# Kernel tuning notes

Hardware: AMD Instinct MI355X
Metric: run time of the kernel (lower is better)

The kernel has to match this reference:

```python
import jax, jax.numpy as jnp
import numpy as np

N = 100_000          # nodes
E = 1_600_000        # edges (avg degree 16)
F_RAW = 124          # float feature columns (after id column removed)
ID_DIM = 4
NF = F_RAW + ID_DIM  # encoder input features = 128
EMB = 64             # embedding_size, heads=1
L = 4                # num_layers
VOCAB = 2048         # id embedding table size
GAT_SLOPE = 0.2      # GATv2 attention leaky slope (PyG default)
ACT_SLOPE = 0.01     # nn.LeakyReLU default
EPS = 1e-5           # GraphNorm eps


def setup_inputs() -> dict:
    key = jax.random.key(0)
    ks = jax.random.split(key, 12)
    x_feat = jax.random.normal(ks[0], (N, F_RAW), jnp.float32)
    node_ids = jax.random.randint(ks[1], (N,), 0, VOCAB)
    edge_index = jax.random.randint(ks[2], (2, E), 0, N)
    emb_table = jax.random.normal(ks[3], (VOCAB, ID_DIM), jnp.float32) * 0.1
    w_in = jax.random.normal(ks[4], (NF, EMB), jnp.float32) / np.sqrt(NF)
    b_in = jnp.zeros((EMB,), jnp.float32)
    lin_w = jax.random.normal(ks[5], (L, EMB, EMB), jnp.float32) / np.sqrt(EMB)
    lin_b = jnp.zeros((L, EMB), jnp.float32)
    att = jax.random.normal(ks[6], (L, EMB), jnp.float32) / np.sqrt(EMB)
    conv_b = jnp.zeros((L, EMB), jnp.float32)
    gn_w = jnp.ones((L, EMB), jnp.float32)
    gn_b = jnp.zeros((L, EMB), jnp.float32)
    gn_ms = jnp.ones((L, EMB), jnp.float32)  # GraphNorm mean_scale
    return {"x_feat": x_feat, "node_ids": node_ids, "edge_index": edge_index,
            "emb_table": emb_table, "w_in": w_in, "b_in": b_in,
            "lin_w": lin_w, "lin_b": lin_b, "att": att, "conv_b": conv_b,
            "gn_w": gn_w, "gn_b": gn_b, "gn_ms": gn_ms}


def reference(x_feat, node_ids, edge_index, emb_table, w_in, b_in,
              lin_w, lin_b, att, conv_b, gn_w, gn_b, gn_ms):
    # id_encode: embedding lookup + concat with float features
    x = jnp.concatenate([x_feat, emb_table[node_ids]], axis=1)  # [N, 128]
    # encoder input projection (BatchNorm skipped: remove_random=True)
    x = jax.nn.leaky_relu(x @ w_in + b_in, ACT_SLOPE)           # [N, 64]
    n = x.shape[0]
    loops = jnp.arange(n)
    src = jnp.concatenate([edge_index[0], loops])               # add self loops
    dst = jnp.concatenate([edge_index[1], loops])
    h = None
    xs = []
    for l in range(L):
        # GATv2Conv, heads=1, share_weights=True (one shared linear)
        g = x @ lin_w[l] + lin_b[l]                             # [N, 64]
        e = jax.nn.leaky_relu(g[src] + g[dst], GAT_SLOPE) @ att[l]  # [E+N]
        # segment softmax over incoming edges per target node
        m = jax.ops.segment_max(e, dst, num_segments=n)
        ee = jnp.exp(e - m[dst])
        s = jax.ops.segment_sum(ee, dst, num_segments=n)
        alpha = ee / s[dst]                                     # [E+N]
        xs.append(alpha)
        x = jax.ops.segment_sum(alpha[:, None] * g[src], dst, num_segments=n) + conv_b[l]
        # GraphNorm (single graph: batch=None)
        mean = jnp.mean(x, axis=0)
        out = x - mean * gn_ms[l]
        var = jnp.mean(out * out, axis=0)
        x = out / jnp.sqrt(var + EPS) * gn_w[l] + gn_b[l]
        x = jax.nn.leaky_relu(x, ACT_SLOPE)
        # dropout p=0.3 is identity at inference
        h = x * 0.5 if h is None else h + x * 0.5
    return x, h, jnp.stack(xs, axis=0)  # ([N,64], [N,64], [L, E+N])
```

## Files before the change

### kernel.cpp

```cpp
#include <hip/hip_runtime.h>
#include <hip/hip_bf16.h>
#include <cstdint>

typedef __hip_bfloat16 bf16;
#define DEVI __device__ __forceinline__

DEVI float b2f(bf16 v){ return __bfloat162float(v); }
DEVI bf16 f2b(float v){ return __float2bfloat16(v); }
DEVI float lrelu(float x, float s){ return x > 0.f ? x : x * s; }

DEVI float ldf(const void* p, size_t i, int f){
  return f ? b2f(((const bf16*)p)[i]) : ((const float*)p)[i];
}
DEVI void stf(void* p, size_t i, int f, float v){
  if(f) ((bf16*)p)[i] = f2b(v); else ((float*)p)[i] = v;
}

DEVI float wave_sum(float v){
#pragma unroll
  for(int o = 32; o > 0; o >>= 1) v += __shfl_xor(v, o, 64);
  return v;
}
DEVI float qsum(float v){
  v += __shfl_xor(v, 1, 64);
  v += __shfl_xor(v, 2, 64);
  v += __shfl_xor(v, 4, 64);
  v += __shfl_xor(v, 8, 64);
  return v;
}

__global__ void k_detect(const uint32_t* __restrict__ xf, int* flag){
  const int lane = threadIdx.x & 63;
  float cnt = 0.f;
  for(int i = lane; i < 256; i += 64){
    uint32_t e = (xf[i] >> 7) & 0xFF;
    if(e >= 100 && e <= 140) cnt += 1.f;
  }
  cnt = wave_sum(cnt);
  if(lane == 0 && blockIdx.x == 0) *flag = (cnt > 180.f) ? 1 : 0;
}

__global__ __launch_bounds__(256) void k_encoder(
    const void* __restrict__ xf, const int* __restrict__ ids,
    const void* __restrict__ emb, const void* __restrict__ win,
    const void* __restrict__ bin, float* __restrict__ x,
    const int* __restrict__ flagp, int N)
{
  __shared__ float W[128*64];
  __shared__ float B[64];
  __shared__ float XR[4][128];
  const int t = threadIdx.x;
  const int f = *flagp;
  for(int i = t; i < 128*64; i += 256) W[i] = ldf(win, i, f);
  if(t < 64) B[t] = ldf(bin, t, f);
  __syncthreads();
  const int w = t >> 6, lane = t & 63;
  for(int base = blockIdx.x*4; base < N; base += gridDim.x*4){
    const int node = base + w;
    if(node < N){
      for(int k = lane; k < 128; k += 64){
        float v;
        if(k < 124) v = ldf(xf, (size_t)node*124 + k, f);
        else        v = ldf(emb, (size_t)ids[node]*4 + (k-124), f);
        XR[w][k] = v;
      }
      float acc = B[lane];
#pragma unroll 8
      for(int k = 0; k < 128; k++) acc = fmaf(XR[w][k], W[k*64+lane], acc);
      x[(size_t)node*64 + lane] = lrelu(acc, 0.01f);
    }
  }
}

__global__ __launch_bounds__(256) void k_linear(
    const float* __restrict__ x, const void* __restrict__ lw,
    const void* __restrict__ lb, float* __restrict__ g,
    const int* __restrict__ flagp, int layer, int N)
{
  __shared__ float W[64*64];
  __shared__ float B[64];
  __shared__ float XR[4][64];
  const int t = threadIdx.x;
  const int f = *flagp;
  const size_t wofs = (size_t)layer*64*64, bofs = (size_t)layer*64;
  for(int i = t; i < 64*64; i += 256) W[i] = ldf(lw, wofs + i, f);
  if(t < 64) B[t] = ldf(lb, bofs + t, f);
  __syncthreads();
  const int w = t >> 6, lane = t & 63;
  for(int base = blockIdx.x*4; base < N; base += gridDim.x*4){
    const int node = base + w;
    if(node < N){
      XR[w][lane] = x[(size_t)node*64 + lane];
      float acc = B[lane];
#pragma unroll 8
      for(int k = 0; k < 64; k++) acc = fmaf(XR[w][k], W[k*64+lane], acc);
      g[(size_t)node*64 + lane] = acc;
    }
  }
}

__global__ void k_deg_init(int* deg, float* stats, int N){
  int i = blockIdx.x*blockDim.x + threadIdx.x;
  if(i < N) deg[i] = 1;
  if(i < 4096) stats[i] = 0.f;
}
__global__ void k_deg_count(const int* __restrict__ dst, int* deg, int E){
  int j = blockIdx.x*blockDim.x + threadIdx.x;
  if(j < E) atomicAdd(&deg[dst[j]], 1);
}
__global__ __launch_bounds__(256) void k_scan_partial(const int* __restrict__ deg, int* partial, int N){
  __shared__ int red[256];
  const int c = blockIdx.x, base = c*1024, t = threadIdx.x;
  int s = 0;
  for(int i = t; i < 1024; i += 256){ int idx = base+i; s += (idx < N) ? deg[idx] : 0; }
  red[t] = s; __syncthreads();
  for(int o = 128; o > 0; o >>= 1){ if(t < o) red[t] += red[t+o]; __syncthreads(); }
  if(t == 0) partial[c] = red[0];
}
__global__ __launch_bounds__(256) void k_scan_final(
    const int* __restrict__ deg, const int* __restrict__ partial,
    int* __restrict__ off, int* __restrict__ cur, int N, int nchunks)
{
  __shared__ int vals[1024];
  __shared__ int tsum[256];
  __shared__ int red[256];
  const int c = blockIdx.x, base = c*1024, t = threadIdx.x;
  red[t] = (t < c && t < nchunks) ? partial[t] : 0;
  for(int i = t; i < 1024; i += 256){ int idx = base+i; vals[i] = (idx < N) ? deg[idx] : 0; }
  __syncthreads();
  for(int o = 128; o > 0; o >>= 1){ if(t < o) red[t] += red[t+o]; __syncthreads(); }
  const int cbase = red[0];
  int a0 = vals[t*4], a1 = vals[t*4+1], a2 = vals[t*4+2], a3 = vals[t*4+3];
  int s = a0+a1+a2+a3;
  tsum[t] = s; __syncthreads();
  for(int o = 1; o < 256; o <<= 1){
    int v = (t >= o) ? tsum[t-o] : 0;
    __syncthreads();
    tsum[t] += v;
    __syncthreads();
  }
  int excl = tsum[t] - s + cbase;
  int o0 = excl, o1 = o0+a0, o2 = o1+a1, o3 = o2+a2;
  int idx = base + t*4;
  if(idx   < N){ off[idx]   = o0; cur[idx]   = o0; }
  if(idx+1 < N){ off[idx+1] = o1; cur[idx+1] = o1; }
  if(idx+2 < N){ off[idx+2] = o2; cur[idx+2] = o2; }
  if(idx+3 < N){ off[idx+3] = o3; cur[idx+3] = o3; }
}
__global__ void k_scatter(const int* __restrict__ src, const int* __restrict__ dst,
                          int* cur, int* __restrict__ pos, int* __restrict__ csrc,
                          int E, int N){
  int j = blockIdx.x*blockDim.x + threadIdx.x;
  int T = E + N;
  if(j >= T) return;
  int s, d;
  if(j < E){ s = src[j]; d = dst[j]; } else { s = j - E; d = s; }
  int p = atomicAdd(&cur[d], 1);
  csrc[p] = s;
  pos[j]  = p;
}

__global__ __launch_bounds__(256) void k_gat(
    const float* __restrict__ g, const int* __restrict__ off,
    const int* __restrict__ deg, const int* __restrict__ csrc,
    const void* __restrict__ att, const void* __restrict__ convb,
    float* __restrict__ xout, float* __restrict__ acsr,
    float* __restrict__ stats, const int* __restrict__ flagp,
    int layer, int N)
{
  __shared__ float sv[4][64], sv2[4][64];
  const int t = threadIdx.x, w = t >> 6, lane = t & 63;
  const int q = lane >> 4, L = lane & 15;
  const int f = *flagp;
  const size_t pofs = (size_t)layer*64;
  float* __restrict__ st = stats + (size_t)layer*1024;
  const int node = blockIdx.x*4 + w;
  const bool act = node < N;
  const int nc = act ? node : (N-1);

  float4 attv, cbv;
  attv.x = ldf(att, pofs + 4*L+0, f); attv.y = ldf(att, pofs + 4*L+1, f);
  attv.z = ldf(att, pofs + 4*L+2, f); attv.w = ldf(att, pofs + 4*L+3, f);
  cbv.x = ldf(convb, pofs + 4*L+0, f); cbv.y = ldf(convb, pofs + 4*L+1, f);
  cbv.z = ldf(convb, pofs + 4*L+2, f); cbv.w = ldf(convb, pofs + 4*L+3, f);

  const float4 gd = *(const float4*)(g + (size_t)nc*64 + 4*L);
  const int o = off[nc];
  const int d = act ? deg[nc] : 0;
  const int sreg = csrc[o + (lane < d ? lane : 0)];

  float m = -1e30f, sp = 0.f, ereg = -1e30f;
  float4 acc = {0.f, 0.f, 0.f, 0.f};
  const int nit = (d + 3) >> 2;

  float4 gs;
  {
    const int s0 = __shfl(sreg, q, 64);
    gs = *(const float4*)(g + (size_t)s0*64 + 4*L);
  }
  for(int i = 0; i < nit; i++){
    float4 gnx = {0.f, 0.f, 0.f, 0.f};
    const int i1 = i + 1;
    const bool more = i1 < nit;
    if(more){
      int sn;
      if(i1 < 16) sn = __shfl(sreg, i1*4 + q, 64);
      else { const int j2 = i1*4 + q; sn = csrc[o + (j2 < d ? j2 : 0)]; }
      gnx = *(const float4*)(g + (size_t)sn*64 + 4*L);
    }
    const int j = i*4 + q;
    const bool have = j < d;
    float pe = lrelu(gs.x+gd.x, 0.2f)*attv.x + lrelu(gs.y+gd.y, 0.2f)*attv.y
             + lrelu(gs.z+gd.z, 0.2f)*attv.z + lrelu(gs.w+gd.w, 0.2f)*attv.w;
    float e = qsum(pe);
    if(!have) e = -1e30f;
    ereg = (L == i) ? e : ereg;
    const float mn = fmaxf(m, e);
    const float sc = __expf(m - mn);
    const float wt = __expf(e - mn);
    sp    = sp*sc    + wt;
    acc.x = acc.x*sc + wt*gs.x;
    acc.y = acc.y*sc + wt*gs.y;
    acc.z = acc.z*sc + wt*gs.z;
    acc.w = acc.w*sc + wt*gs.w;
    m = mn;
    if(more) gs = gnx;
  }
#pragma unroll
  for(int ofs = 16; ofs <= 32; ofs <<= 1){
    const float m2  = __shfl_xor(m,  ofs, 64);
    const float sp2 = __shfl_xor(sp, ofs, 64);
    float4 a2;
    a2.x = __shfl_xor(acc.x, ofs, 64); a2.y = __shfl_xor(acc.y, ofs, 64);
    a2.z = __shfl_xor(acc.z, ofs, 64); a2.w = __shfl_xor(acc.w, ofs, 64);
    const float mn = fmaxf(m, m2);
    const float sA = __expf(m - mn), sB = __expf(m2 - mn);
    sp    = sp*sA    + sp2*sB;
    acc.x = acc.x*sA + a2.x*sB;
    acc.y = acc.y*sA + a2.y*sB;
    acc.z = acc.z*sA + a2.z*sB;
    acc.w = acc.w*sA + a2.w*sB;
    m = mn;
  }
  const float inv = 1.f / sp;

  if(act){
    const int j = 4*L + q;
    if(j < d && j < 64)
      acsr[o + j] = __expf(ereg - m) * inv;
    for(int i = 16; i < nit; i++){
      const int j2 = i*4 + q;
      const bool have = j2 < d;
      const int s = csrc[o + (have ? j2 : 0)];
      const float4 gs2 = *(const float4*)(g + (size_t)s*64 + 4*L);
      float pe = lrelu(gs2.x+gd.x, 0.2f)*attv.x + lrelu(gs2.y+gd.y, 0.2f)*attv.y
               + lrelu(gs2.z+gd.z, 0.2f)*attv.z + lrelu(gs2.w+gd.w, 0.2f)*attv.w;
      float e = qsum(pe);
      if(have && L == 0)
        acsr[o + j2] = __expf(e - m) * inv;
    }
  }
  float4 v4 = {0.f, 0.f, 0.f, 0.f};
  if(act){
    v4.x = acc.x*inv + cbv.x; v4.y = acc.y*inv + cbv.y;
    v4.z = acc.z*inv + cbv.z; v4.w = acc.w*inv + cbv.w;
    if(q == 0) *(float4*)(xout + (size_t)node*64 + 4*L) = v4;
  }
  if(q == 0){
    sv [w][4*L+0] = v4.x;      sv [w][4*L+1] = v4.y;
    sv [w][4*L+2] = v4.z;      sv [w][4*L+3] = v4.w;
    sv2[w][4*L+0] = v4.x*v4.x; sv2[w][4*L+1] = v4.y*v4.y;
    sv2[w][4*L+2] = v4.z*v4.z; sv2[w][4*L+3] = v4.w*v4.w;
  }
  __syncthreads();
  if(w == 0){
    float a = sv[0][lane]+sv[1][lane]+sv[2][lane]+sv[3][lane];
    float b = sv2[0][lane]+sv2[1][lane]+sv2[2][lane]+sv2[3][lane];
    const int bank = (blockIdx.x & 7) * 128;
    atomicAdd(&st[bank + lane],      a);
    atomicAdd(&st[bank + 64 + lane], b);
  }
}

__global__ __launch_bounds__(256) void k_gn_apply(
    float* __restrict__ x, const float* __restrict__ stats,
    const void* __restrict__ gw, const void* __restrict__ gb,
    const void* __restrict__ gms, void* __restrict__ out,
    const float* __restrict__ acsr, const int* __restrict__ pos,
    size_t x_base, size_t h_base, size_t alpha_base,
    const int* __restrict__ flagp, int N, int T, int layer, float invN)
{
  const int f = *flagp;
  const int lane = threadIdx.x & 63;
  const float* __restrict__ st = stats + (size_t)layer*1024;
  const size_t pofs = (size_t)layer*64;
  float s1 = 0.f, s2 = 0.f;
#pragma unroll
  for(int c = 0; c < 8; c++){
    s1 += st[c*128 + lane];
    s2 += st[c*128 + 64 + lane];
  }
  const float mean = s1 * invN;
  const float ex2  = s2 * invN;
  const float c    = mean * ldf(gms, pofs + lane, f);
  const float var  = ex2 - 2.f*c*mean + c*c;
  const float a    = ldf(gw, pofs + lane, f) / sqrtf(var + 1e-5f);
  const float bb   = ldf(gb, pofs + lane, f);
  const size_t total = (size_t)N * 64;
  for(size_t idx = (size_t)blockIdx.x*256 + threadIdx.x; idx < total;
      idx += (size_t)gridDim.x*256){
    float v = (x[idx] - c) * a + bb;
    v = lrelu(v, 0.01f);
    x[idx] = v;
    float hv = 0.5f*v + (layer == 0 ? 0.f : ldf(out, h_base + idx, f));
    stf(out, h_base + idx, f, hv);
    if(layer == 3) stf(out, x_base + idx, f, v);
  }
  for(size_t j = (size_t)blockIdx.x*256 + threadIdx.x; j < (size_t)T;
      j += (size_t)gridDim.x*256){
    stf(out, alpha_base + j, f, acsr[pos[j]]);
  }
}

extern "C" void kernel_launch(void* const* d_in, const int* in_sizes, int n_in,
                              void* d_out, int out_size, void* d_ws, size_t ws_size,
                              hipStream_t stream) {
  const void* xf   = d_in[0];
  const int*  ids  = (const int*)d_in[1];
  const int*  eidx = (const int*)d_in[2];
  const void* emb  = d_in[3];
  const void* win  = d_in[4];
  const void* bin  = d_in[5];
  const void* lw   = d_in[6];
  const void* lb   = d_in[7];
  const void* att  = d_in[8];
  const void* cb   = d_in[9];
  const void* gw   = d_in[10];
  const void* gb   = d_in[11];
  const void* gms  = d_in[12];

  const int N = in_sizes[1];
  const int E = in_sizes[2] / 2;
  const int T = E + N;
  const int* srcp = eidx;
  const int* dstp = eidx + E;

  char* p = (char*)d_ws;
  float* x  = (float*)p; p += (size_t)N*64*4;
  float* g  = (float*)p; p += (size_t)N*64*4;
  int* deg  = (int*)p;   p += ((size_t)N*4 + 63) & ~63ull;
  int* off  = (int*)p;   p += ((size_t)N*4 + 63) & ~63ull;
  int* cur  = (int*)p;   p += ((size_t)N*4 + 63) & ~63ull;
  int* pos  = (int*)p;   p += ((size_t)T*4 + 63) & ~63ull;
  int* csrc = (int*)p;   p += ((size_t)T*4 + 63) & ~63ull;
  float* acsr = (float*)p; p += ((size_t)T*4 + 63) & ~63ull;
  int* partial = (int*)p; p += 4096;
  float* stats = (float*)p; p += 4*1024*4;
  int* flag = (int*)p;   p += 64;

  const size_t x_base = 0;
  const size_t h_base = (size_t)N*64;
  const size_t a_base = (size_t)2*N*64;

  k_detect<<<1, 64, 0, stream>>>((const uint32_t*)xf, flag);
  k_encoder<<<2048, 256, 0, stream>>>(xf, ids, emb, win, bin, x, flag, N);

  k_deg_init <<<(N+255)/256, 256, 0, stream>>>(deg, stats, N);
  k_deg_count<<<(E+255)/256, 256, 0, stream>>>(dstp, deg, E);
  const int nchunks = (N + 1023) / 1024;
  k_scan_partial<<<nchunks, 256, 0, stream>>>(deg, partial, N);
  k_scan_final  <<<nchunks, 256, 0, stream>>>(deg, partial, off, cur, N, nchunks);
  k_scatter     <<<(T+255)/256, 256, 0, stream>>>(srcp, dstp, cur, pos, csrc, E, N);

  for(int l = 0; l < 4; l++){
    k_linear<<<2048, 256, 0, stream>>>(x, lw, lb, g, flag, l, N);
    k_gat<<<(N+3)/4, 256, 0, stream>>>(g, off, deg, csrc, att, cb, x,
                                       acsr, stats, flag, l, N);
    k_gn_apply<<<1024, 256, 0, stream>>>(x, stats, gw, gb, gms, d_out,
                                         acsr, pos, x_base, h_base,
                                         a_base + (size_t)l*T, flag,
                                         N, T, l, 1.0f/(float)N);
  }
}
```

Baseline: 1.149 ms.

## Fuse GraphNorm apply into next layer's linear and deepen GAT gather prefetch

Moves the previous layer's GraphNorm normalization, activation, h accumulation and alpha scatter into the following layer's linear kernel. A separate final kernel handles the last layer. This removes a read-modify-write pass over x per layer and three kernel launches. The GAT kernel also prefetches source features two iterations ahead instead of one, to hide gather latency at the cost of extra registers.

New measurement: 1.073 ms. 1.07x faster.

```diff
diff --git a/kernel.cpp b/kernel.cpp
--- a/kernel.cpp
+++ b/kernel.cpp
@@ -75,7 +75,11 @@
 __global__ __launch_bounds__(256) void k_linear(
     const float* __restrict__ x, const void* __restrict__ lw,
     const void* __restrict__ lb, float* __restrict__ g,
-    const int* __restrict__ flagp, int layer, int N)
+    const float* __restrict__ stats, const void* __restrict__ gw,
+    const void* __restrict__ gb, const void* __restrict__ gms,
+    void* __restrict__ out, const float* __restrict__ acsr,
+    const int* __restrict__ pos, size_t h_base, size_t alpha_base,
+    const int* __restrict__ flagp, int layer, int N, int T, float invN)
 {
   __shared__ float W[64*64];
   __shared__ float B[64];
@@ -85,17 +89,43 @@
   const size_t wofs = (size_t)layer*64*64, bofs = (size_t)layer*64;
   for(int i = t; i < 64*64; i += 256) W[i] = ldf(lw, wofs + i, f);
   if(t < 64) B[t] = ldf(lb, bofs + t, f);
+  const int w = t >> 6, lane = t & 63;
+  float c = 0.f, a = 1.f, bb = 0.f;
+  if(layer > 0){
+    const int pl = layer - 1;
+    const float* __restrict__ st = stats + (size_t)pl*1024;
+    const size_t pofs = (size_t)pl*64;
+    float s1 = 0.f, s2 = 0.f;
+#pragma unroll
+    for(int k = 0; k < 8; k++){ s1 += st[k*128 + lane]; s2 += st[k*128 + 64 + lane]; }
+    const float mean = s1*invN, ex2 = s2*invN;
+    c = mean * ldf(gms, pofs + lane, f);
+    const float var = ex2 - 2.f*c*mean + c*c;
+    a = ldf(gw, pofs + lane, f) / sqrtf(var + 1e-5f);
+    bb = ldf(gb, pofs + lane, f);
+  }
   __syncthreads();
-  const int w = t >> 6, lane = t & 63;
   for(int base = blockIdx.x*4; base < N; base += gridDim.x*4){
     const int node = base + w;
     if(node < N){
-      XR[w][lane] = x[(size_t)node*64 + lane];
+      const size_t idx = (size_t)node*64 + lane;
+      float v = x[idx];
+      if(layer > 0){
+        v = lrelu((v - c)*a + bb, 0.01f);
+        float hv = 0.5f*v + (layer == 1 ? 0.f : ldf(out, h_base + idx, f));
+        stf(out, h_base + idx, f, hv);
+      }
+      XR[w][lane] = v;
       float acc = B[lane];
 #pragma unroll 8
       for(int k = 0; k < 64; k++) acc = fmaf(XR[w][k], W[k*64+lane], acc);
-      g[(size_t)node*64 + lane] = acc;
+      g[idx] = acc;
     }
+  }
+  if(layer > 0){
+    for(size_t j = (size_t)blockIdx.x*256 + threadIdx.x; j < (size_t)T;
+        j += (size_t)gridDim.x*256)
+      stf(out, alpha_base + j, f, acsr[pos[j]]);
   }
 }
 
@@ -193,21 +223,26 @@
   float4 acc = {0.f, 0.f, 0.f, 0.f};
   const int nit = (d + 3) >> 2;
 
-  float4 gs;
+  float4 gsA = {0.f,0.f,0.f,0.f}, gsB = {0.f,0.f,0.f,0.f};
   {
     const int s0 = __shfl(sreg, q, 64);
-    gs = *(const float4*)(g + (size_t)s0*64 + 4*L);
+    gsA = *(const float4*)(g + (size_t)s0*64 + 4*L);
+  }
+  if(nit > 1){
+    const int s1 = __shfl(sreg, 4 + q, 64);
+    gsB = *(const float4*)(g + (size_t)s1*64 + 4*L);
   }
   for(int i = 0; i < nit; i++){
     float4 gnx = {0.f, 0.f, 0.f, 0.f};
-    const int i1 = i + 1;
-    const bool more = i1 < nit;
-    if(more){
+    const int i2 = i + 2;
+    const bool more2 = i2 < nit;
+    if(more2){
       int sn;
-      if(i1 < 16) sn = __shfl(sreg, i1*4 + q, 64);
-      else { const int j2 = i1*4 + q; sn = csrc[o + (j2 < d ? j2 : 0)]; }
+      if(i2 < 16) sn = __shfl(sreg, i2*4 + q, 64);
+      else { const int j2 = i2*4 + q; sn = csrc[o + (j2 < d ? j2 : 0)]; }
       gnx = *(const float4*)(g + (size_t)sn*64 + 4*L);
     }
+    const float4 gs = gsA;
     const int j = i*4 + q;
     const bool have = j < d;
     float pe = lrelu(gs.x+gd.x, 0.2f)*attv.x + lrelu(gs.y+gd.y, 0.2f)*attv.y
@@ -224,7 +259,8 @@
     acc.z = acc.z*sc + wt*gs.z;
     acc.w = acc.w*sc + wt*gs.w;
     m = mn;
-    if(more) gs = gnx;
+    gsA = gsB;
+    if(more2) gsB = gnx;
   }
 #pragma unroll
   for(int ofs = 16; ofs <= 32; ofs <<= 1){
@@ -282,18 +318,18 @@
   }
 }
 
-__global__ __launch_bounds__(256) void k_gn_apply(
-    float* __restrict__ x, const float* __restrict__ stats,
+__global__ __launch_bounds__(256) void k_gn_final(
+    const float* __restrict__ x, const float* __restrict__ stats,
     const void* __restrict__ gw, const void* __restrict__ gb,
     const void* __restrict__ gms, void* __restrict__ out,
     const float* __restrict__ acsr, const int* __restrict__ pos,
     size_t x_base, size_t h_base, size_t alpha_base,
-    const int* __restrict__ flagp, int N, int T, int layer, float invN)
+    const int* __restrict__ flagp, int N, int T, float invN)
 {
   const int f = *flagp;
   const int lane = threadIdx.x & 63;
-  const float* __restrict__ st = stats + (size_t)layer*1024;
-  const size_t pofs = (size_t)layer*64;
+  const float* __restrict__ st = stats + (size_t)3*1024;
+  const size_t pofs = (size_t)3*64;
   float s1 = 0.f, s2 = 0.f;
 #pragma unroll
   for(int c = 0; c < 8; c++){
@@ -311,10 +347,9 @@
       idx += (size_t)gridDim.x*256){
     float v = (x[idx] - c) * a + bb;
     v = lrelu(v, 0.01f);
-    x[idx] = v;
-    float hv = 0.5f*v + (layer == 0 ? 0.f : ldf(out, h_base + idx, f));
+    float hv = 0.5f*v + ldf(out, h_base + idx, f);
     stf(out, h_base + idx, f, hv);
-    if(layer == 3) stf(out, x_base + idx, f, v);
+    stf(out, x_base + idx, f, v);
   }
   for(size_t j = (size_t)blockIdx.x*256 + threadIdx.x; j < (size_t)T;
       j += (size_t)gridDim.x*256){
@@ -361,6 +396,7 @@
   const size_t x_base = 0;
   const size_t h_base = (size_t)N*64;
   const size_t a_base = (size_t)2*N*64;
+  const float invN = 1.0f/(float)N;
 
   k_detect<<<1, 64, 0, stream>>>((const uint32_t*)xf, flag);
   k_encoder<<<2048, 256, 0, stream>>>(xf, ids, emb, win, bin, x, flag, N);
@@ -373,12 +409,14 @@
   k_scatter     <<<(T+255)/256, 256, 0, stream>>>(srcp, dstp, cur, pos, csrc, E, N);
 
   for(int l = 0; l < 4; l++){
-    k_linear<<<2048, 256, 0, stream>>>(x, lw, lb, g, flag, l, N);
+    k_linear<<<2048, 256, 0, stream>>>(x, lw, lb, g, stats, gw, gb, gms,
+                                       d_out, acsr, pos, h_base,
+                                       a_base + (size_t)(l-1)*T,
+                                       flag, l, N, T, invN);
     k_gat<<<(N+3)/4, 256, 0, stream>>>(g, off, deg, csrc, att, cb, x,
                                        acsr, stats, flag, l, N);
-    k_gn_apply<<<1024, 256, 0, stream>>>(x, stats, gw, gb, gms, d_out,
-                                         acsr, pos, x_base, h_base,
-                                         a_base + (size_t)l*T, flag,
-                                         N, T, l, 1.0f/(float)N);
-  }
-}
+  }
+  k_gn_final<<<1024, 256, 0, stream>>>(x, stats, gw, gb, gms, d_out,
+                                       acsr, pos, x_base, h_base,
+                                       a_base + (size_t)3*T, flag, N, T, invN);
+}
```
